# Kernel optimization log

Hardware: AMD Instinct MI355X
Metric: run time of the kernel (lower is better)

Reference implementation:

```python
import jax, jax.numpy as jnp
import numpy as np

N_NODES = 50000
N_EDGES = 1_600_000
D = 128


def setup_inputs() -> dict:
    key = jax.random.key(0)
    k1, k2, k3 = jax.random.split(key, 3)
    x = jax.random.normal(k1, (N_NODES, D), dtype=jnp.float32)
    edge_index = jax.random.randint(k2, (2, N_EDGES), 0, N_NODES, dtype=jnp.int64)
    W = jax.random.normal(k3, (D, D), dtype=jnp.float32) / np.sqrt(D)
    b = jnp.zeros((D,), dtype=jnp.float32)
    return {"x": x, "edge_index": edge_index, "W": W, "b": b}


def _sgconv(x, src, dst, W, b, n):
    # gcn_norm with self-loops: D^{-1/2} (A + I) D^{-1/2}
    loop = jnp.arange(n, dtype=src.dtype)
    src = jnp.concatenate([src, loop])
    dst = jnp.concatenate([dst, loop])
    ones = jnp.ones(src.shape[0], dtype=x.dtype)
    deg = jax.ops.segment_sum(ones, dst, num_segments=n)  # in-degree incl. self-loop
    dinv = jnp.where(deg > 0, jax.lax.rsqrt(deg), jnp.zeros_like(deg))
    norm = dinv[src] * dinv[dst]                      # [E+N]
    msg = x[src] * norm[:, None]                      # gather + scale, [E+N, D]
    agg = jax.ops.segment_sum(msg, dst, num_segments=n)  # scatter-add, [N, D]
    return agg @ W.T + b                              # SGConv linear (K=1)


def reference(x, edge_index, W, b):
    n = x.shape[0]
    h = _sgconv(x, edge_index[0], edge_index[1], W, b, n)
    return x + jax.nn.relu(h)
```

## Files before the change

kernel.cpp:

```cpp
#include <hip/hip_runtime.h>
#include <hip/hip_fp16.h>

#define D 128
#define BSHIFT 6
#define BSIZE 64
#define NBMAX 1024
#define BCAP 3072
#define CPAD 16
#define PREP_BLOCKS 256
#define OVF_CAP 65536
#define GB_THREADS 1024


using half8 = __attribute__((ext_vector_type(8))) _Float16;
using float4v = __attribute__((ext_vector_type(4))) float;
using floatx2 = __attribute__((ext_vector_type(2))) float;

__global__ __launch_bounds__(256) void prep_kernel(const int* __restrict__ src,
                                                   const int* __restrict__ dst,
                                                   int* __restrict__ bucket_cnt,
                                                   int* __restrict__ pairs,
                                                   int* __restrict__ ovfA_cnt,
                                                   int2* __restrict__ ovfA,
                                                   int E, int NB) {
    __shared__ int sbase[NBMAX];
    __shared__ int cur[NBMAX];
    const int t = threadIdx.x;
    for (int b = t; b < NB; b += 256) { sbase[b] = 0; cur[b] = 0; }
    __syncthreads();

    int chunk = (((E + (int)gridDim.x - 1) / (int)gridDim.x) + 3) & ~3;
    int start = blockIdx.x * chunk;
    int end = min(start + chunk, E);

    for (int i = start + 4 * t; i < end; i += 4 * 256) {
        if (i + 3 < end) {
            int4 v = *(const int4*)&dst[i];
            atomicAdd(&sbase[v.x >> BSHIFT], 1);
            atomicAdd(&sbase[v.y >> BSHIFT], 1);
            atomicAdd(&sbase[v.z >> BSHIFT], 1);
            atomicAdd(&sbase[v.w >> BSHIFT], 1);
        } else {
            for (int j = i; j < end; ++j) atomicAdd(&sbase[dst[j] >> BSHIFT], 1);
        }
    }
    __syncthreads();

    for (int b = t; b < NB; b += 256) {
        int h = sbase[b];
        sbase[b] = h ? atomicAdd(&bucket_cnt[b * CPAD], h) : 0;
    }
    __syncthreads();

    auto place = [&](int dd, int ss) {
        int b = dd >> BSHIFT;
        int p = sbase[b] + atomicAdd(&cur[b], 1);
        if (p < BCAP) {
            pairs[(size_t)b * BCAP + p] = (ss << BSHIFT) | (dd & (BSIZE - 1));
        } else {
            int q = atomicAdd(ovfA_cnt, 1);
            if (q < OVF_CAP) ovfA[q] = make_int2(dd, ss);
        }
    };

    for (int i = start + 4 * t; i < end; i += 4 * 256) {
        if (i + 3 < end) {
            int4 dv = *(const int4*)&dst[i];
            int4 sv = *(const int4*)&src[i];
            place(dv.x, sv.x);
            place(dv.y, sv.y);
            place(dv.z, sv.z);
            place(dv.w, sv.w);
        } else {
            for (int j = i; j < end; ++j) place(dst[j], src[j]);
        }
    }
}

__global__ __launch_bounds__(256) void xw_kernel(const float* __restrict__ x,
                                                 const float* __restrict__ W,
                                                 const int* __restrict__ pairs,
                                                 const int* __restrict__ bucket_cnt,
                                                 const int* __restrict__ ovfA_cnt,
                                                 const int2* __restrict__ ovfA,
                                                 unsigned char* __restrict__ xw, int N) {
    __shared__ _Float16 Bf[128 * 128];
    __shared__ int degX[BSIZE];
    const int t = threadIdx.x;
    const int b = blockIdx.x;
    if (t < BSIZE) degX[t] = 0;
    __syncthreads();

    {
        int cnt = min(bucket_cnt[b * CPAD], BCAP);
        const int* pp = pairs + (size_t)b * BCAP;
        for (int i = t; i < cnt; i += 256) atomicAdd(&degX[pp[i] & (BSIZE - 1)], 1);
        int na = *ovfA_cnt;
        if (na > 0) {
            if (na > OVF_CAP) na = OVF_CAP;
            for (int k = t; k < na; k += 256) {
                int dd = ovfA[k].x;
                if ((dd >> BSHIFT) == b) atomicAdd(&degX[dd & (BSIZE - 1)], 1);
            }
        }
    }

    {
        int n = t >> 1;
        int jt = n >> 4, nlo = n & 15;
        int kbase = (t & 1) * 64;
#pragma unroll
        for (int o = 0; o < 8; ++o) {
            int k0 = kbase + o * 8;
            float4 f0 = *(const float4*)&W[n * 128 + k0];
            float4 f1 = *(const float4*)&W[n * 128 + k0 + 4];
            int kt = k0 >> 5, quad = (k0 >> 3) & 3;
            half8 h;
            h[0] = (_Float16)f0.x; h[1] = (_Float16)f0.y;
            h[2] = (_Float16)f0.z; h[3] = (_Float16)f0.w;
            h[4] = (_Float16)f1.x; h[5] = (_Float16)f1.y;
            h[6] = (_Float16)f1.z; h[7] = (_Float16)f1.w;
            *(half8*)&Bf[(size_t)(((kt * 8 + jt) * 4 + quad) * 16 + nlo) * 8] = h;
        }
    }
    __syncthreads();

    const int wave = t >> 6, lane = t & 63;
    const int quad = lane >> 4, nlo = lane & 15;
    const int r0 = b * 64 + wave * 16;
    const int rA = r0 + nlo;
    const int rAc = (rA < N) ? rA : (N - 1);
    const float dv = rsqrtf((float)degX[rAc - b * 64] + 1.0f);

    float4v acc[8];
#pragma unroll
    for (int j = 0; j < 8; ++j) acc[j] = (float4v){0.f, 0.f, 0.f, 0.f};

#pragma unroll
    for (int kt = 0; kt < 4; ++kt) {
        const float* xp = x + (size_t)rAc * D + kt * 32 + quad * 8;
        float4 a0 = *(const float4*)xp;
        float4 a1 = *(const float4*)(xp + 4);
        half8 va;
        va[0] = (_Float16)(a0.x * dv); va[1] = (_Float16)(a0.y * dv);
        va[2] = (_Float16)(a0.z * dv); va[3] = (_Float16)(a0.w * dv);
        va[4] = (_Float16)(a1.x * dv); va[5] = (_Float16)(a1.y * dv);
        va[6] = (_Float16)(a1.z * dv); va[7] = (_Float16)(a1.w * dv);
#pragma unroll
        for (int jt = 0; jt < 8; ++jt) {
            half8 vb = *(half8*)&Bf[(size_t)((kt * 8 + jt) * 64 + lane) * 8];
            acc[jt] = __builtin_amdgcn_mfma_f32_16x16x32_f16(va, vb, acc[jt], 0, 0, 0);
        }
    }

#pragma unroll
    for (int reg = 0; reg < 4; ++reg) {
        int row = r0 + quad * 4 + reg;
        if (row < N) {
            int u0 = __builtin_amdgcn_cvt_pk_fp8_f32(acc[0][reg], acc[1][reg], 0, false);
            u0 = __builtin_amdgcn_cvt_pk_fp8_f32(acc[2][reg], acc[3][reg], u0, true);
            int u1 = __builtin_amdgcn_cvt_pk_fp8_f32(acc[4][reg], acc[5][reg], 0, false);
            u1 = __builtin_amdgcn_cvt_pk_fp8_f32(acc[6][reg], acc[7][reg], u1, true);
            *(uint2*)(xw + (size_t)row * 128 + nlo * 8) = make_uint2((unsigned)u0, (unsigned)u1);
        }
    }
}

__global__ __launch_bounds__(GB_THREADS) void gatherB_kernel(
    const float* __restrict__ x, const unsigned char* __restrict__ xw,
    const int* __restrict__ pairs, const int* __restrict__ bucket_cnt,
    const float* __restrict__ bias, const int* __restrict__ ovfA_cnt,
    const int2* __restrict__ ovfA, float* __restrict__ out, int N) {
    __shared__ int lds_src[BCAP];
    __shared__ int degL[BSIZE], offs[BSIZE], cur[BSIZE], spillc[BSIZE];
    const int b = blockIdx.x;
    const int t = threadIdx.x;
    if (t < BSIZE) { degL[t] = 0; cur[t] = 0; spillc[t] = 0; }
    __syncthreads();
    const int cnt = min(bucket_cnt[b * CPAD], BCAP);
    int na = *ovfA_cnt;
    if (na > OVF_CAP) na = OVF_CAP;

    const int* slab = pairs + (size_t)b * BCAP;
    int w0 = 0, w1 = 0, w2 = 0;
    const bool p0 = t < cnt, p1 = t + 1024 < cnt, p2 = t + 2048 < cnt;
    if (p0) { w0 = slab[t];        atomicAdd(&degL[w0 & (BSIZE - 1)], 1); }
    if (p1) { w1 = slab[t + 1024]; atomicAdd(&degL[w1 & (BSIZE - 1)], 1); }
    if (p2) { w2 = slab[t + 2048]; atomicAdd(&degL[w2 & (BSIZE - 1)], 1); }
    if (na > 0) {
        for (int k = t; k < na; k += GB_THREADS) {
            int dd = ovfA[k].x;
            if ((dd >> BSHIFT) == b) atomicAdd(&spillc[dd & (BSIZE - 1)], 1);
        }
    }
    __syncthreads();

    if (t < BSIZE) {
        int v = degL[t];
        int s = v;
#pragma unroll
        for (int o = 1; o < 64; o <<= 1) {
            int u = __shfl_up(s, o, 64);
            if (t >= o) s += u;
        }
        offs[t] = s - v;
    }
    __syncthreads();

    if (p0) { int dl = w0 & (BSIZE - 1); lds_src[offs[dl] + atomicAdd(&cur[dl], 1)] = w0 >> BSHIFT; }
    if (p1) { int dl = w1 & (BSIZE - 1); lds_src[offs[dl] + atomicAdd(&cur[dl], 1)] = w1 >> BSHIFT; }
    if (p2) { int dl = w2 & (BSIZE - 1); lds_src[offs[dl] + atomicAdd(&cur[dl], 1)] = w2 >> BSHIFT; }
    __syncthreads();

    const int wave = t >> 6, lane = t & 63;
    const int g = lane >> 4, c15 = lane & 15;
    const uint2* xw64 = (const uint2*)xw;

    const int sb0 = c15 * 8 + 2 * g, sb1 = sb0 + 1;
    const int colA = ((sb0 & 7) << 4) + (sb0 >> 3);
    const int colB = ((sb1 & 7) << 4) + (sb1 >> 3);
    const float bA = bias[colA], bB = bias[colB];

    for (int q = 0; q < 4; ++q) {
        int dl = wave * 4 + q;
        int node = b * BSIZE + dl;
        if (node >= N) break;
        int start = offs[dl];
        int end = start + degL[dl];
        float dvd = rsqrtf((float)(degL[dl] + spillc[dl]) + 1.0f);
        size_t noff = (size_t)node * D;

        float a0 = 0.f, a1 = 0.f, a2 = 0.f, a3 = 0.f;
        float a4 = 0.f, a5 = 0.f, a6 = 0.f, a7 = 0.f;

#define ACC8(v)                                                              \
    {                                                                        \
        floatx2 q0 = __builtin_amdgcn_cvt_pk_f32_fp8((int)(v).x, false);     \
        floatx2 q1 = __builtin_amdgcn_cvt_pk_f32_fp8((int)(v).x, true);      \
        floatx2 q2 = __builtin_amdgcn_cvt_pk_f32_fp8((int)(v).y, false);     \
        floatx2 q3 = __builtin_amdgcn_cvt_pk_f32_fp8((int)(v).y, true);      \
        a0 += q0.x; a1 += q0.y; a2 += q1.x; a3 += q1.y;                      \
        a4 += q2.x; a5 += q2.y; a6 += q3.x; a7 += q3.y;                      \
    }

        int e = start;
        for (; e + 15 < end; e += 16) {
            int r0 = lds_src[e + 0 + g], r1 = lds_src[e + 4 + g];
            int r2 = lds_src[e + 8 + g], r3 = lds_src[e + 12 + g];
            uint2 v0 = xw64[(size_t)r0 * 16 + c15];
            uint2 v1 = xw64[(size_t)r1 * 16 + c15];
            uint2 v2 = xw64[(size_t)r2 * 16 + c15];
            uint2 v3 = xw64[(size_t)r3 * 16 + c15];
            ACC8(v0) ACC8(v1) ACC8(v2) ACC8(v3)
        }
        for (; e < end; e += 4) {
            int idx = e + g;
            uint2 v = make_uint2(0u, 0u);
            if (idx < end) {
                int r = lds_src[idx];
                v = xw64[(size_t)r * 16 + c15];
            }
            ACC8(v)
        }

        a0 += __shfl_xor(a0, 16); a0 += __shfl_xor(a0, 32);
        a1 += __shfl_xor(a1, 16); a1 += __shfl_xor(a1, 32);
        a2 += __shfl_xor(a2, 16); a2 += __shfl_xor(a2, 32);
        a3 += __shfl_xor(a3, 16); a3 += __shfl_xor(a3, 32);
        a4 += __shfl_xor(a4, 16); a4 += __shfl_xor(a4, 32);
        a5 += __shfl_xor(a5, 16); a5 += __shfl_xor(a5, 32);
        a6 += __shfl_xor(a6, 16); a6 += __shfl_xor(a6, 32);
        a7 += __shfl_xor(a7, 16); a7 += __shfl_xor(a7, 32);

        {
            uint2 vs = xw64[(size_t)node * 16 + c15];
            ACC8(vs)
            if (na > 0) {
                for (int k = 0; k < na; ++k) {
                    int2 pr = ovfA[k];
                    if (pr.x == node) {
                        uint2 v = xw64[(size_t)pr.y * 16 + c15];
                        ACC8(v)
                    }
                }
            }
        }
#undef ACC8

        float sA = (g == 0) ? a0 : (g == 1) ? a2 : (g == 2) ? a4 : a6;
        float sB = (g == 0) ? a1 : (g == 1) ? a3 : (g == 2) ? a5 : a7;
        float hA = sA * dvd + bA;
        float hB = sB * dvd + bB;
        out[noff + colA] = x[noff + colA] + (hA > 0.f ? hA : 0.f);
        out[noff + colB] = x[noff + colB] + (hB > 0.f ? hB : 0.f);
    }
}

extern "C" void kernel_launch(void* const* d_in, const int* in_sizes, int n_in,
                              void* d_out, int out_size, void* d_ws, size_t ws_size,
                              hipStream_t stream) {
    const float* x = (const float*)d_in[0];
    const int* ei = (const int*)d_in[1];
    const float* W = (const float*)d_in[2];
    const float* bias = (const float*)d_in[3];
    float* out = (float*)d_out;

    const int N = in_sizes[0] / D;
    const int E = in_sizes[1] / 2;
    const int* src = ei;
    const int* dst = ei + E;
    const int NB = (N + BSIZE - 1) / BSIZE;

    char* p = (char*)d_ws;
    int* pairs = (int*)p;            p += (size_t)NB * BCAP * sizeof(int);
    unsigned char* xw = (unsigned char*)p; p += (size_t)N * 128;
    int* bucket_cnt = (int*)p;       p += (size_t)NBMAX * CPAD * sizeof(int);
    int* ovfA_cnt = (int*)p;         p += 16;
    int2* ovfA = (int2*)p;           p += (size_t)OVF_CAP * sizeof(int2);

    hipMemsetAsync(bucket_cnt, 0, (size_t)NBMAX * CPAD * sizeof(int) + 16, stream);

    prep_kernel<<<PREP_BLOCKS, 256, 0, stream>>>(src, dst, bucket_cnt, pairs,
                                                 ovfA_cnt, ovfA, E, NB);
    xw_kernel<<<NB, 256, 0, stream>>>(x, W, pairs, bucket_cnt, ovfA_cnt, ovfA, xw, N);
    gatherB_kernel<<<NB, GB_THREADS, 0, stream>>>(x, xw, pairs, bucket_cnt,
                                                  bias, ovfA_cnt, ovfA, out, N);
}
```

Before: 159.2 us.

## Overlap edge bucketing with x·W GEMM by moving source normalization into gather

The x·W transform no longer depends on node degrees, so it runs in the same launch as the edge-bucketing prep blocks and the two can overlap. A small dinv kernel builds a per-node rsqrt(degree) table. The gather kernel then scales each neighbor's fp8 row by that table value, stored next to the source index in LDS as an int2. This removes the serial dependency between bucketing and the GEMM. In exchange it adds a launch, doubles LDS for the edge list, adds a multiply per element in the gather loop, and does a random global read of dinv per edge.

```diff
diff --git a/kernel.cpp b/kernel.cpp
--- a/kernel.cpp
+++ b/kernel.cpp
@@ -16,153 +16,160 @@
 using float4v = __attribute__((ext_vector_type(4))) float;
 using floatx2 = __attribute__((ext_vector_type(2))) float;
 
-__global__ __launch_bounds__(256) void prep_kernel(const int* __restrict__ src,
-                                                   const int* __restrict__ dst,
-                                                   int* __restrict__ bucket_cnt,
-                                                   int* __restrict__ pairs,
-                                                   int* __restrict__ ovfA_cnt,
-                                                   int2* __restrict__ ovfA,
-                                                   int E, int NB) {
-    __shared__ int sbase[NBMAX];
-    __shared__ int cur[NBMAX];
+__global__ __launch_bounds__(256) void fused_kernel(const int* __restrict__ src,
+                                                    const int* __restrict__ dst,
+                                                    const float* __restrict__ x,
+                                                    const float* __restrict__ W,
+                                                    int* __restrict__ bucket_cnt,
+                                                    int* __restrict__ pairs,
+                                                    int* __restrict__ ovfA_cnt,
+                                                    int2* __restrict__ ovfA,
+                                                    unsigned char* __restrict__ xw,
+                                                    int E, int NB, int N) {
+    __shared__ __align__(16) char smem_raw[32768];
     const int t = threadIdx.x;
-    for (int b = t; b < NB; b += 256) { sbase[b] = 0; cur[b] = 0; }
-    __syncthreads();
-
-    int chunk = (((E + (int)gridDim.x - 1) / (int)gridDim.x) + 3) & ~3;
-    int start = blockIdx.x * chunk;
-    int end = min(start + chunk, E);
-
-    for (int i = start + 4 * t; i < end; i += 4 * 256) {
-        if (i + 3 < end) {
-            int4 v = *(const int4*)&dst[i];
-            atomicAdd(&sbase[v.x >> BSHIFT], 1);
-            atomicAdd(&sbase[v.y >> BSHIFT], 1);
-            atomicAdd(&sbase[v.z >> BSHIFT], 1);
-            atomicAdd(&sbase[v.w >> BSHIFT], 1);
-        } else {
-            for (int j = i; j < end; ++j) atomicAdd(&sbase[dst[j] >> BSHIFT], 1);
-        }
-    }
-    __syncthreads();
-
-    for (int b = t; b < NB; b += 256) {
-        int h = sbase[b];
-        sbase[b] = h ? atomicAdd(&bucket_cnt[b * CPAD], h) : 0;
-    }
-    __syncthreads();
-
-    auto place = [&](int dd, int ss) {
-        int b = dd >> BSHIFT;
-        int p = sbase[b] + atomicAdd(&cur[b], 1);
-        if (p < BCAP) {
-            pairs[(size_t)b * BCAP + p] = (ss << BSHIFT) | (dd & (BSIZE - 1));
-        } else {
-            int q = atomicAdd(ovfA_cnt, 1);
-            if (q < OVF_CAP) ovfA[q] = make_int2(dd, ss);
-        }
-    };
-
-    for (int i = start + 4 * t; i < end; i += 4 * 256) {
-        if (i + 3 < end) {
-            int4 dv = *(const int4*)&dst[i];
-            int4 sv = *(const int4*)&src[i];
-            place(dv.x, sv.x);
-            place(dv.y, sv.y);
-            place(dv.z, sv.z);
-            place(dv.w, sv.w);
-        } else {
-            for (int j = i; j < end; ++j) place(dst[j], src[j]);
+
+    if (blockIdx.x < PREP_BLOCKS) {
+        int* sbase = (int*)smem_raw;
+        int* cur = sbase + NBMAX;
+        for (int b = t; b < NB; b += 256) { sbase[b] = 0; cur[b] = 0; }
+        __syncthreads();
+
+        int chunk = (((E + PREP_BLOCKS - 1) / PREP_BLOCKS) + 3) & ~3;
+        int start = blockIdx.x * chunk;
+        int end = min(start + chunk, E);
+
+        for (int i = start + 4 * t; i < end; i += 4 * 256) {
+            if (i + 3 < end) {
+                int4 v = *(const int4*)&dst[i];
+                atomicAdd(&sbase[v.x >> BSHIFT], 1);
+                atomicAdd(&sbase[v.y >> BSHIFT], 1);
+                atomicAdd(&sbase[v.z >> BSHIFT], 1);
+                atomicAdd(&sbase[v.w >> BSHIFT], 1);
+            } else {
+                for (int j = i; j < end; ++j) atomicAdd(&sbase[dst[j] >> BSHIFT], 1);
+            }
+        }
+        __syncthreads();
+
+        for (int b = t; b < NB; b += 256) {
+            int h = sbase[b];
+            sbase[b] = h ? atomicAdd(&bucket_cnt[b * CPAD], h) : 0;
+        }
+        __syncthreads();
+
+        auto place = [&](int dd, int ss) {
+            int b = dd >> BSHIFT;
+            int p = sbase[b] + atomicAdd(&cur[b], 1);
+            if (p < BCAP) {
+                pairs[(size_t)b * BCAP + p] = (ss << BSHIFT) | (dd & (BSIZE - 1));
+            } else {
+                int q = atomicAdd(ovfA_cnt, 1);
+                if (q < OVF_CAP) ovfA[q] = make_int2(dd, ss);
+            }
+        };
+        for (int i = start + 4 * t; i < end; i += 4 * 256) {
+            if (i + 3 < end) {
+                int4 dv = *(const int4*)&dst[i];
+                int4 sv = *(const int4*)&src[i];
+                place(dv.x, sv.x);
+                place(dv.y, sv.y);
+                place(dv.z, sv.z);
+                place(dv.w, sv.w);
+            } else {
+                for (int j = i; j < end; ++j) place(dst[j], src[j]);
+            }
+        }
+    } else {
+        const int b = blockIdx.x - PREP_BLOCKS;
+        _Float16* Bf = (_Float16*)smem_raw;
+
+        {
+            int n = t >> 1;
+            int jt = n >> 4, nlo = n & 15;
+            int kbase = (t & 1) * 64;
+#pragma unroll
+            for (int o = 0; o < 8; ++o) {
+                int k0 = kbase + o * 8;
+                float4 f0 = *(const float4*)&W[n * 128 + k0];
+                float4 f1 = *(const float4*)&W[n * 128 + k0 + 4];
+                int kt = k0 >> 5, quad = (k0 >> 3) & 3;
+                half8 h;
+                h[0] = (_Float16)f0.x; h[1] = (_Float16)f0.y;
+                h[2] = (_Float16)f0.z; h[3] = (_Float16)f0.w;
+                h[4] = (_Float16)f1.x; h[5] = (_Float16)f1.y;
+                h[6] = (_Float16)f1.z; h[7] = (_Float16)f1.w;
+                *(half8*)&Bf[(size_t)(((kt * 8 + jt) * 4 + quad) * 16 + nlo) * 8] = h;
+            }
+        }
+        __syncthreads();
+
+        const int lane = t & 63;
+        const int quad = lane >> 4, nlo = lane & 15;
+        const int r0 = b * 64 + (t >> 6) * 16;
+        const int rA = r0 + nlo;
+        const int rAc = (rA < N) ? rA : (N - 1);
+
+        float4v acc[8];
+#pragma unroll
+        for (int j = 0; j < 8; ++j) acc[j] = (float4v){0.f, 0.f, 0.f, 0.f};
+
+#pragma unroll
+        for (int kt = 0; kt < 4; ++kt) {
+            const float* xp = x + (size_t)rAc * D + kt * 32 + quad * 8;
+            float4 a0 = *(const float4*)xp;
+            float4 a1 = *(const float4*)(xp + 4);
+            half8 va;
+            va[0] = (_Float16)a0.x; va[1] = (_Float16)a0.y;
+            va[2] = (_Float16)a0.z; va[3] = (_Float16)a0.w;
+            va[4] = (_Float16)a1.x; va[5] = (_Float16)a1.y;
+            va[6] = (_Float16)a1.z; va[7] = (_Float16)a1.w;
+#pragma unroll
+            for (int jt = 0; jt < 8; ++jt) {
+                half8 vb = *(half8*)&Bf[(size_t)((kt * 8 + jt) * 64 + lane) * 8];
+                acc[jt] = __builtin_amdgcn_mfma_f32_16x16x32_f16(va, vb, acc[jt], 0, 0, 0);
+            }
+        }
+
+#pragma unroll
+        for (int reg = 0; reg < 4; ++reg) {
+            int row = r0 + quad * 4 + reg;
+            if (row < N) {
+                int u0 = __builtin_amdgcn_cvt_pk_fp8_f32(acc[0][reg], acc[1][reg], 0, false);
+                u0 = __builtin_amdgcn_cvt_pk_fp8_f32(acc[2][reg], acc[3][reg], u0, true);
+                int u1 = __builtin_amdgcn_cvt_pk_fp8_f32(acc[4][reg], acc[5][reg], 0, false);
+                u1 = __builtin_amdgcn_cvt_pk_fp8_f32(acc[6][reg], acc[7][reg], u1, true);
+                *(uint2*)(xw + (size_t)row * 128 + nlo * 8) = make_uint2((unsigned)u0, (unsigned)u1);
+            }
         }
     }
 }
 
-__global__ __launch_bounds__(256) void xw_kernel(const float* __restrict__ x,
-                                                 const float* __restrict__ W,
-                                                 const int* __restrict__ pairs,
-                                                 const int* __restrict__ bucket_cnt,
-                                                 const int* __restrict__ ovfA_cnt,
-                                                 const int2* __restrict__ ovfA,
-                                                 unsigned char* __restrict__ xw, int N) {
-    __shared__ _Float16 Bf[128 * 128];
+__global__ __launch_bounds__(256) void dinv_kernel(const int* __restrict__ pairs,
+                                                   const int* __restrict__ bucket_cnt,
+                                                   const int* __restrict__ ovfA_cnt,
+                                                   const int2* __restrict__ ovfA,
+                                                   float* __restrict__ dinvTab, int N) {
     __shared__ int degX[BSIZE];
     const int t = threadIdx.x;
     const int b = blockIdx.x;
     if (t < BSIZE) degX[t] = 0;
     __syncthreads();
-
-    {
-        int cnt = min(bucket_cnt[b * CPAD], BCAP);
-        const int* pp = pairs + (size_t)b * BCAP;
-        for (int i = t; i < cnt; i += 256) atomicAdd(&degX[pp[i] & (BSIZE - 1)], 1);
-        int na = *ovfA_cnt;
-        if (na > 0) {
-            if (na > OVF_CAP) na = OVF_CAP;
-            for (int k = t; k < na; k += 256) {
-                int dd = ovfA[k].x;
-                if ((dd >> BSHIFT) == b) atomicAdd(&degX[dd & (BSIZE - 1)], 1);
-            }
-        }
-    }
-
-    {
-        int n = t >> 1;
-        int jt = n >> 4, nlo = n & 15;
-        int kbase = (t & 1) * 64;
-#pragma unroll
-        for (int o = 0; o < 8; ++o) {
-            int k0 = kbase + o * 8;
-            float4 f0 = *(const float4*)&W[n * 128 + k0];
-            float4 f1 = *(const float4*)&W[n * 128 + k0 + 4];
-            int kt = k0 >> 5, quad = (k0 >> 3) & 3;
-            half8 h;
-            h[0] = (_Float16)f0.x; h[1] = (_Float16)f0.y;
-            h[2] = (_Float16)f0.z; h[3] = (_Float16)f0.w;
-            h[4] = (_Float16)f1.x; h[5] = (_Float16)f1.y;
-            h[6] = (_Float16)f1.z; h[7] = (_Float16)f1.w;
-            *(half8*)&Bf[(size_t)(((kt * 8 + jt) * 4 + quad) * 16 + nlo) * 8] = h;
-        }
-    }
-    __syncthreads();
-
-    const int wave = t >> 6, lane = t & 63;
-    const int quad = lane >> 4, nlo = lane & 15;
-    const int r0 = b * 64 + wave * 16;
-    const int rA = r0 + nlo;
-    const int rAc = (rA < N) ? rA : (N - 1);
-    const float dv = rsqrtf((float)degX[rAc - b * 64] + 1.0f);
-
-    float4v acc[8];
-#pragma unroll
-    for (int j = 0; j < 8; ++j) acc[j] = (float4v){0.f, 0.f, 0.f, 0.f};
-
-#pragma unroll
-    for (int kt = 0; kt < 4; ++kt) {
-        const float* xp = x + (size_t)rAc * D + kt * 32 + quad * 8;
-        float4 a0 = *(const float4*)xp;
-        float4 a1 = *(const float4*)(xp + 4);
-        half8 va;
-        va[0] = (_Float16)(a0.x * dv); va[1] = (_Float16)(a0.y * dv);
-        va[2] = (_Float16)(a0.z * dv); va[3] = (_Float16)(a0.w * dv);
-        va[4] = (_Float16)(a1.x * dv); va[5] = (_Float16)(a1.y * dv);
-        va[6] = (_Float16)(a1.z * dv); va[7] = (_Float16)(a1.w * dv);
-#pragma unroll
-        for (int jt = 0; jt < 8; ++jt) {
-            half8 vb = *(half8*)&Bf[(size_t)((kt * 8 + jt) * 64 + lane) * 8];
-            acc[jt] = __builtin_amdgcn_mfma_f32_16x16x32_f16(va, vb, acc[jt], 0, 0, 0);
-        }
-    }
-
-#pragma unroll
-    for (int reg = 0; reg < 4; ++reg) {
-        int row = r0 + quad * 4 + reg;
-        if (row < N) {
-            int u0 = __builtin_amdgcn_cvt_pk_fp8_f32(acc[0][reg], acc[1][reg], 0, false);
-            u0 = __builtin_amdgcn_cvt_pk_fp8_f32(acc[2][reg], acc[3][reg], u0, true);
-            int u1 = __builtin_amdgcn_cvt_pk_fp8_f32(acc[4][reg], acc[5][reg], 0, false);
-            u1 = __builtin_amdgcn_cvt_pk_fp8_f32(acc[6][reg], acc[7][reg], u1, true);
-            *(uint2*)(xw + (size_t)row * 128 + nlo * 8) = make_uint2((unsigned)u0, (unsigned)u1);
-        }
+    int cnt = min(bucket_cnt[b * CPAD], BCAP);
+    const int* pp = pairs + (size_t)b * BCAP;
+    for (int i = t; i < cnt; i += 256) atomicAdd(&degX[pp[i] & (BSIZE - 1)], 1);
+    int na = *ovfA_cnt;
+    if (na > 0) {
+        if (na > OVF_CAP) na = OVF_CAP;
+        for (int k = t; k < na; k += 256) {
+            int dd = ovfA[k].x;
+            if ((dd >> BSHIFT) == b) atomicAdd(&degX[dd & (BSIZE - 1)], 1);
+        }
+    }
+    __syncthreads();
+    if (t < BSIZE) {
+        int node = b * BSIZE + t;
+        if (node < N) dinvTab[node] = rsqrtf((float)degX[t] + 1.0f);
     }
 }
 
@@ -170,8 +177,9 @@
     const float* __restrict__ x, const unsigned char* __restrict__ xw,
     const int* __restrict__ pairs, const int* __restrict__ bucket_cnt,
     const float* __restrict__ bias, const int* __restrict__ ovfA_cnt,
-    const int2* __restrict__ ovfA, float* __restrict__ out, int N) {
-    __shared__ int lds_src[BCAP];
+    const int2* __restrict__ ovfA, const float* __restrict__ dinvTab,
+    float* __restrict__ out, int N) {
+    __shared__ int2 lds2[BCAP];
     __shared__ int degL[BSIZE], offs[BSIZE], cur[BSIZE], spillc[BSIZE];
     const int b = blockIdx.x;
     const int t = threadIdx.x;
@@ -183,10 +191,11 @@
 
     const int* slab = pairs + (size_t)b * BCAP;
     int w0 = 0, w1 = 0, w2 = 0;
+    float s0f = 0.f, s1f = 0.f, s2f = 0.f;
     const bool p0 = t < cnt, p1 = t + 1024 < cnt, p2 = t + 2048 < cnt;
-    if (p0) { w0 = slab[t];        atomicAdd(&degL[w0 & (BSIZE - 1)], 1); }
-    if (p1) { w1 = slab[t + 1024]; atomicAdd(&degL[w1 & (BSIZE - 1)], 1); }
-    if (p2) { w2 = slab[t + 2048]; atomicAdd(&degL[w2 & (BSIZE - 1)], 1); }
+    if (p0) { w0 = slab[t];        atomicAdd(&degL[w0 & (BSIZE - 1)], 1); s0f = dinvTab[w0 >> BSHIFT]; }
+    if (p1) { w1 = slab[t + 1024]; atomicAdd(&degL[w1 & (BSIZE - 1)], 1); s1f = dinvTab[w1 >> BSHIFT]; }
+    if (p2) { w2 = slab[t + 2048]; atomicAdd(&degL[w2 & (BSIZE - 1)], 1); s2f = dinvTab[w2 >> BSHIFT]; }
     if (na > 0) {
         for (int k = t; k < na; k += GB_THREADS) {
             int dd = ovfA[k].x;
@@ -207,9 +216,9 @@
     }
     __syncthreads();
 
-    if (p0) { int dl = w0 & (BSIZE - 1); lds_src[offs[dl] + atomicAdd(&cur[dl], 1)] = w0 >> BSHIFT; }
-    if (p1) { int dl = w1 & (BSIZE - 1); lds_src[offs[dl] + atomicAdd(&cur[dl], 1)] = w1 >> BSHIFT; }
-    if (p2) { int dl = w2 & (BSIZE - 1); lds_src[offs[dl] + atomicAdd(&cur[dl], 1)] = w2 >> BSHIFT; }
+    if (p0) { int dl = w0 & (BSIZE - 1); lds2[offs[dl] + atomicAdd(&cur[dl], 1)] = make_int2(w0 >> BSHIFT, __float_as_int(s0f)); }
+    if (p1) { int dl = w1 & (BSIZE - 1); lds2[offs[dl] + atomicAdd(&cur[dl], 1)] = make_int2(w1 >> BSHIFT, __float_as_int(s1f)); }
+    if (p2) { int dl = w2 & (BSIZE - 1); lds2[offs[dl] + atomicAdd(&cur[dl], 1)] = make_int2(w2 >> BSHIFT, __float_as_int(s2f)); }
     __syncthreads();
 
     const int wave = t >> 6, lane = t & 63;
@@ -233,34 +242,39 @@
         float a0 = 0.f, a1 = 0.f, a2 = 0.f, a3 = 0.f;
         float a4 = 0.f, a5 = 0.f, a6 = 0.f, a7 = 0.f;
 
-#define ACC8(v)                                                              \
+#define ACC8(v, s)                                                           \
     {                                                                        \
         floatx2 q0 = __builtin_amdgcn_cvt_pk_f32_fp8((int)(v).x, false);     \
         floatx2 q1 = __builtin_amdgcn_cvt_pk_f32_fp8((int)(v).x, true);      \
         floatx2 q2 = __builtin_amdgcn_cvt_pk_f32_fp8((int)(v).y, false);     \
         floatx2 q3 = __builtin_amdgcn_cvt_pk_f32_fp8((int)(v).y, true);      \
-        a0 += q0.x; a1 += q0.y; a2 += q1.x; a3 += q1.y;                      \
-        a4 += q2.x; a5 += q2.y; a6 += q3.x; a7 += q3.y;                      \
+        a0 += q0.x * (s); a1 += q0.y * (s); a2 += q1.x * (s); a3 += q1.y * (s); \
+        a4 += q2.x * (s); a5 += q2.y * (s); a6 += q3.x * (s); a7 += q3.y * (s); \
     }
 
         int e = start;
         for (; e + 15 < end; e += 16) {
-            int r0 = lds_src[e + 0 + g], r1 = lds_src[e + 4 + g];
-            int r2 = lds_src[e + 8 + g], r3 = lds_src[e + 12 + g];
-            uint2 v0 = xw64[(size_t)r0 * 16 + c15];
-            uint2 v1 = xw64[(size_t)r1 * 16 + c15];
-            uint2 v2 = xw64[(size_t)r2 * 16 + c15];
-            uint2 v3 = xw64[(size_t)r3 * 16 + c15];
-            ACC8(v0) ACC8(v1) ACC8(v2) ACC8(v3)
+            int2 e0 = lds2[e + 0 + g], e1 = lds2[e + 4 + g];
+            int2 e2 = lds2[e + 8 + g], e3 = lds2[e + 12 + g];
+            uint2 v0 = xw64[(size_t)e0.x * 16 + c15];
+            uint2 v1 = xw64[(size_t)e1.x * 16 + c15];
+            uint2 v2 = xw64[(size_t)e2.x * 16 + c15];
+            uint2 v3 = xw64[(size_t)e3.x * 16 + c15];
+            ACC8(v0, __int_as_float(e0.y))
+            ACC8(v1, __int_as_float(e1.y))
+            ACC8(v2, __int_as_float(e2.y))
+            ACC8(v3, __int_as_float(e3.y))
         }
         for (; e < end; e += 4) {
             int idx = e + g;
             uint2 v = make_uint2(0u, 0u);
+            float s = 0.f;
             if (idx < end) {
-                int r = lds_src[idx];
-                v = xw64[(size_t)r * 16 + c15];
-            }
-            ACC8(v)
+                int2 pr = lds2[idx];
+                v = xw64[(size_t)pr.x * 16 + c15];
+                s = __int_as_float(pr.y);
+            }
+            ACC8(v, s)
         }
 
         a0 += __shfl_xor(a0, 16); a0 += __shfl_xor(a0, 32);
@@ -274,13 +288,13 @@
 
         {
             uint2 vs = xw64[(size_t)node * 16 + c15];
-            ACC8(vs)
+            ACC8(vs, dvd)
             if (na > 0) {
                 for (int k = 0; k < na; ++k) {
                     int2 pr = ovfA[k];
                     if (pr.x == node) {
                         uint2 v = xw64[(size_t)pr.y * 16 + c15];
-                        ACC8(v)
+                        ACC8(v, dinvTab[pr.y])
                     }
                 }
             }
@@ -317,12 +331,14 @@
     int* bucket_cnt = (int*)p;       p += (size_t)NBMAX * CPAD * sizeof(int);
     int* ovfA_cnt = (int*)p;         p += 16;
     int2* ovfA = (int2*)p;           p += (size_t)OVF_CAP * sizeof(int2);
+    float* dinvTab = (float*)p;      p += (size_t)NBMAX * BSIZE * sizeof(float);
 
     hipMemsetAsync(bucket_cnt, 0, (size_t)NBMAX * CPAD * sizeof(int) + 16, stream);
 
-    prep_kernel<<<PREP_BLOCKS, 256, 0, stream>>>(src, dst, bucket_cnt, pairs,
-                                                 ovfA_cnt, ovfA, E, NB);
-    xw_kernel<<<NB, 256, 0, stream>>>(x, W, pairs, bucket_cnt, ovfA_cnt, ovfA, xw, N);
+    fused_kernel<<<PREP_BLOCKS + NB, 256, 0, stream>>>(src, dst, x, W, bucket_cnt,
+                                                       pairs, ovfA_cnt, ovfA, xw,
+                                                       E, NB, N);
+    dinv_kernel<<<NB, 256, 0, stream>>>(pairs, bucket_cnt, ovfA_cnt, ovfA, dinvTab, N);
     gatherB_kernel<<<NB, GB_THREADS, 0, stream>>>(x, xw, pairs, bucket_cnt,
-                                                  bias, ovfA_cnt, ovfA, out, N);
+                                                  bias, ovfA_cnt, ovfA, dinvTab, out, N);
 }
```

Result: slower. 174.0 us (+9.3%).

## Make xw kernel persistent, reusing LDS-converted W across bucket pairs

Applied to the files above, without the earlier changes.

The xw kernel now launches a fixed grid of 256 blocks with 512 threads, each looping over pairs of buckets. Each 256-thread half handles one bucket per iteration, and the fp16 copy of W is built in LDS once per block rather than once per bucket. This cuts redundant W loads and conversions, but leaves an uneven tail: some blocks run two iterations and others one, and it adds extra block-wide barriers per iteration.

```diff
diff --git a/kernel.cpp b/kernel.cpp
--- a/kernel.cpp
+++ b/kernel.cpp
@@ -10,6 +10,8 @@
 #define PREP_BLOCKS 256
 #define OVF_CAP 65536
 #define GB_THREADS 1024
+#define XW_BLOCKS 256
+#define XW_THREADS 512
 
 
 using half8 = __attribute__((ext_vector_type(8))) _Float16;
@@ -77,40 +79,21 @@
     }
 }
 
-__global__ __launch_bounds__(256) void xw_kernel(const float* __restrict__ x,
-                                                 const float* __restrict__ W,
-                                                 const int* __restrict__ pairs,
-                                                 const int* __restrict__ bucket_cnt,
-                                                 const int* __restrict__ ovfA_cnt,
-                                                 const int2* __restrict__ ovfA,
-                                                 unsigned char* __restrict__ xw, int N) {
+__global__ __launch_bounds__(XW_THREADS) void xw_kernel(
+    const float* __restrict__ x, const float* __restrict__ W,
+    const int* __restrict__ pairs, const int* __restrict__ bucket_cnt,
+    const int* __restrict__ ovfA_cnt, const int2* __restrict__ ovfA,
+    unsigned char* __restrict__ xw, int N, int NB) {
     __shared__ _Float16 Bf[128 * 128];
-    __shared__ int degX[BSIZE];
+    __shared__ int degX[2 * BSIZE];
     const int t = threadIdx.x;
-    const int b = blockIdx.x;
-    if (t < BSIZE) degX[t] = 0;
-    __syncthreads();
 
     {
-        int cnt = min(bucket_cnt[b * CPAD], BCAP);
-        const int* pp = pairs + (size_t)b * BCAP;
-        for (int i = t; i < cnt; i += 256) atomicAdd(&degX[pp[i] & (BSIZE - 1)], 1);
-        int na = *ovfA_cnt;
-        if (na > 0) {
-            if (na > OVF_CAP) na = OVF_CAP;
-            for (int k = t; k < na; k += 256) {
-                int dd = ovfA[k].x;
-                if ((dd >> BSHIFT) == b) atomicAdd(&degX[dd & (BSIZE - 1)], 1);
-            }
-        }
-    }
-
-    {
-        int n = t >> 1;
+        int n = t >> 2;
         int jt = n >> 4, nlo = n & 15;
-        int kbase = (t & 1) * 64;
-#pragma unroll
-        for (int o = 0; o < 8; ++o) {
+        int kbase = (t & 3) * 32;
+#pragma unroll
+        for (int o = 0; o < 4; ++o) {
             int k0 = kbase + o * 8;
             float4 f0 = *(const float4*)&W[n * 128 + k0];
             float4 f1 = *(const float4*)&W[n * 128 + k0 + 4];
@@ -123,46 +106,77 @@
             *(half8*)&Bf[(size_t)(((kt * 8 + jt) * 4 + quad) * 16 + nlo) * 8] = h;
         }
     }
-    __syncthreads();
-
-    const int wave = t >> 6, lane = t & 63;
+
+    const int sub = t >> 8;
+    const int ht = t & 255;
+    const int lane = t & 63;
     const int quad = lane >> 4, nlo = lane & 15;
-    const int r0 = b * 64 + wave * 16;
-    const int rA = r0 + nlo;
-    const int rAc = (rA < N) ? rA : (N - 1);
-    const float dv = rsqrtf((float)degX[rAc - b * 64] + 1.0f);
-
-    float4v acc[8];
-#pragma unroll
-    for (int j = 0; j < 8; ++j) acc[j] = (float4v){0.f, 0.f, 0.f, 0.f};
-
-#pragma unroll
-    for (int kt = 0; kt < 4; ++kt) {
-        const float* xp = x + (size_t)rAc * D + kt * 32 + quad * 8;
-        float4 a0 = *(const float4*)xp;
-        float4 a1 = *(const float4*)(xp + 4);
-        half8 va;
-        va[0] = (_Float16)(a0.x * dv); va[1] = (_Float16)(a0.y * dv);
-        va[2] = (_Float16)(a0.z * dv); va[3] = (_Float16)(a0.w * dv);
-        va[4] = (_Float16)(a1.x * dv); va[5] = (_Float16)(a1.y * dv);
-        va[6] = (_Float16)(a1.z * dv); va[7] = (_Float16)(a1.w * dv);
-#pragma unroll
-        for (int jt = 0; jt < 8; ++jt) {
-            half8 vb = *(half8*)&Bf[(size_t)((kt * 8 + jt) * 64 + lane) * 8];
-            acc[jt] = __builtin_amdgcn_mfma_f32_16x16x32_f16(va, vb, acc[jt], 0, 0, 0);
-        }
-    }
-
-#pragma unroll
-    for (int reg = 0; reg < 4; ++reg) {
-        int row = r0 + quad * 4 + reg;
-        if (row < N) {
-            int u0 = __builtin_amdgcn_cvt_pk_fp8_f32(acc[0][reg], acc[1][reg], 0, false);
-            u0 = __builtin_amdgcn_cvt_pk_fp8_f32(acc[2][reg], acc[3][reg], u0, true);
-            int u1 = __builtin_amdgcn_cvt_pk_fp8_f32(acc[4][reg], acc[5][reg], 0, false);
-            u1 = __builtin_amdgcn_cvt_pk_fp8_f32(acc[6][reg], acc[7][reg], u1, true);
-            *(uint2*)(xw + (size_t)row * 128 + nlo * 8) = make_uint2((unsigned)u0, (unsigned)u1);
-        }
+    const int wv = ht >> 6;
+
+    int na = *ovfA_cnt;
+    if (na > OVF_CAP) na = OVF_CAP;
+
+    const int npairs = (NB + 1) >> 1;
+    for (int bb = blockIdx.x; bb < npairs; bb += XW_BLOCKS) {
+        const int b = 2 * bb + sub;
+        const bool valid = (b < NB);
+        if (ht < BSIZE) degX[sub * BSIZE + ht] = 0;
+        __syncthreads();
+
+        if (valid) {
+            int cnt = min(bucket_cnt[b * CPAD], BCAP);
+            const int* pp = pairs + (size_t)b * BCAP;
+            int* dg = degX + sub * BSIZE;
+            for (int i = ht; i < cnt; i += 256) atomicAdd(&dg[pp[i] & (BSIZE - 1)], 1);
+            if (na > 0) {
+                for (int k = ht; k < na; k += 256) {
+                    int dd = ovfA[k].x;
+                    if ((dd >> BSHIFT) == b) atomicAdd(&dg[dd & (BSIZE - 1)], 1);
+                }
+            }
+        }
+        __syncthreads();
+
+        if (valid) {
+            const int r0 = b * 64 + wv * 16;
+            const int rA = r0 + nlo;
+            const int rAc = (rA < N) ? rA : (N - 1);
+            const float dv = rsqrtf((float)degX[sub * BSIZE + (rAc - b * 64)] + 1.0f);
+
+            float4v acc[8];
+#pragma unroll
+            for (int j = 0; j < 8; ++j) acc[j] = (float4v){0.f, 0.f, 0.f, 0.f};
+
+#pragma unroll
+            for (int kt = 0; kt < 4; ++kt) {
+                const float* xp = x + (size_t)rAc * D + kt * 32 + quad * 8;
+                float4 a0 = *(const float4*)xp;
+                float4 a1 = *(const float4*)(xp + 4);
+                half8 va;
+                va[0] = (_Float16)(a0.x * dv); va[1] = (_Float16)(a0.y * dv);
+                va[2] = (_Float16)(a0.z * dv); va[3] = (_Float16)(a0.w * dv);
+                va[4] = (_Float16)(a1.x * dv); va[5] = (_Float16)(a1.y * dv);
+                va[6] = (_Float16)(a1.z * dv); va[7] = (_Float16)(a1.w * dv);
+#pragma unroll
+                for (int jt = 0; jt < 8; ++jt) {
+                    half8 vb = *(half8*)&Bf[(size_t)((kt * 8 + jt) * 64 + lane) * 8];
+                    acc[jt] = __builtin_amdgcn_mfma_f32_16x16x32_f16(va, vb, acc[jt], 0, 0, 0);
+                }
+            }
+
+#pragma unroll
+            for (int reg = 0; reg < 4; ++reg) {
+                int row = r0 + quad * 4 + reg;
+                if (row < N) {
+                    int u0 = __builtin_amdgcn_cvt_pk_fp8_f32(acc[0][reg], acc[1][reg], 0, false);
+                    u0 = __builtin_amdgcn_cvt_pk_fp8_f32(acc[2][reg], acc[3][reg], u0, true);
+                    int u1 = __builtin_amdgcn_cvt_pk_fp8_f32(acc[4][reg], acc[5][reg], 0, false);
+                    u1 = __builtin_amdgcn_cvt_pk_fp8_f32(acc[6][reg], acc[7][reg], u1, true);
+                    *(uint2*)(xw + (size_t)row * 128 + nlo * 8) = make_uint2((unsigned)u0, (unsigned)u1);
+                }
+            }
+        }
+        __syncthreads();
     }
 }
 
@@ -322,7 +336,8 @@
 
     prep_kernel<<<PREP_BLOCKS, 256, 0, stream>>>(src, dst, bucket_cnt, pairs,
                                                  ovfA_cnt, ovfA, E, NB);
-    xw_kernel<<<NB, 256, 0, stream>>>(x, W, pairs, bucket_cnt, ovfA_cnt, ovfA, xw, N);
+    xw_kernel<<<XW_BLOCKS, XW_THREADS, 0, stream>>>(x, W, pairs, bucket_cnt,
+                                                    ovfA_cnt, ovfA, xw, N, NB);
     gatherB_kernel<<<NB, GB_THREADS, 0, stream>>>(x, xw, pairs, bucket_cnt,
                                                   bias, ovfA_cnt, ovfA, out, N);
 }
```

After: 158.6 us. Within noise of the previous version (-0.4%).
